# Kernel tuning notes

Hardware: AMD Instinct MI355X
Metric: run time of the kernel (lower is better)

The kernel has to match this reference:

```python
import jax, jax.numpy as jnp
import numpy as np

MARGIN = 2.0


def setup_inputs() -> dict:
    key = jax.random.key(0)
    k1, k2 = jax.random.split(key)
    predict = jax.random.normal(k1, (8192, 2048, 1, 1), dtype=jnp.float32)
    gt = jax.random.randint(k2, (8192, 1), 0, 751, dtype=jnp.int64)
    return {"predict": predict, "gt": gt}


def reference(predict, gt):
    # predict: [B, 2048, 1, 1] -> [B, D]
    p = predict.reshape(predict.shape[0], -1)
    b, d = p.shape
    # pairwise squared L2 distance / dim, via GEMM (||a||^2 + ||b||^2 - 2 a.b)
    sq = jnp.sum(p * p, axis=1)  # [B]
    d2 = (sq[:, None] + sq[None, :] - 2.0 * (p @ p.T))
    d2 = jnp.maximum(d2, 0.0) / d  # clamp tiny negatives from GEMM roundoff
    g = gt.reshape(-1)
    label = (g[:, None] == g[None, :]).astype(p.dtype)  # [B, B]
    term = label * d2 + (1.0 - label) * jax.nn.relu(MARGIN - d2)
    # original loop sums over j >= i (diagonal contributes 0: same label, dist 0)
    mask = jnp.triu(jnp.ones((b, b), dtype=bool))
    loss = jnp.sum(jnp.where(mask, term, 0.0))
    return 2.0 * loss / (b * (b - 1))
```

## Files before the change

### kernel.cpp

```cpp
#include <hip/hip_runtime.h>
#include <stdint.h>

#define NROWS 8192
#define DIM   2048
#define MARGIN 2.0f
#define SCALEQ (127.0f / 6.0f)
#define S2     ((6.0f / 127.0f) * (6.0f / 127.0f))

#define BT2     256
#define BKB     128
#define NKT     (DIM / BKB)
#define NT2     (NROWS / BT2)
#define NTILES2 (NT2 * (NT2 + 1) / 2)
#define NSPL    16
#define ABUF_B  32768
#define BUF_B   65536
#define HALF_B  16384

typedef __attribute__((ext_vector_type(4)))  int  int4v;
typedef __attribute__((ext_vector_type(16))) int  int16v;
typedef unsigned char uchar;

__device__ __forceinline__ void decode_tile(int bid, int* ti, int* tj) {
    float fn = (float)NT2 + 0.5f;
    int r = (int)(fn - sqrtf(fn * fn - 2.0f * (float)bid));
    if (r < 0) r = 0;
    if (r >= NT2) r = NT2 - 1;
    while ((r + 1) * NT2 - ((r + 1) * r) / 2 <= bid) ++r;
    while (r * NT2 - (r * (r - 1)) / 2 > bid) --r;
    *ti = r;
    *tj = r + (bid - (r * NT2 - (r * (r - 1)) / 2));
}

__device__ __forceinline__ uint pack4(float4 v) {
    int q0 = (int)__builtin_rintf(v.x * SCALEQ);
    int q1 = (int)__builtin_rintf(v.y * SCALEQ);
    int q2 = (int)__builtin_rintf(v.z * SCALEQ);
    int q3 = (int)__builtin_rintf(v.w * SCALEQ);
    q0 = min(max(q0, -127), 127); q1 = min(max(q1, -127), 127);
    q2 = min(max(q2, -127), 127); q3 = min(max(q3, -127), 127);
    return (uint)(q0 & 0xFF) | ((uint)(q1 & 0xFF) << 8) |
           ((uint)(q2 & 0xFF) << 16) | ((uint)(q3 & 0xFF) << 24);
}

__global__ __launch_bounds__(256) void prep_kernel(const float* __restrict__ p,
                                                   uchar* __restrict__ pb,
                                                   float* __restrict__ sq) {
    int row = blockIdx.x;
    int t = threadIdx.x;
    const float4* prow = (const float4*)(p + (size_t)row * DIM);
    uint* qrow = (uint*)(pb + (size_t)row * DIM);
    float4 a = prow[t];
    float4 b = prow[t + 256];
    float s = a.x * a.x + a.y * a.y + a.z * a.z + a.w * a.w
            + b.x * b.x + b.y * b.y + b.z * b.z + b.w * b.w;
    qrow[t] = pack4(a);
    qrow[t + 256] = pack4(b);
#pragma unroll
    for (int o = 32; o > 0; o >>= 1) s += __shfl_down(s, o, 64);
    __shared__ float wsums[4];
    int lane = t & 63, wvv = t >> 6;
    if (lane == 0) wsums[wvv] = s;
    __syncthreads();
    if (t == 0) sq[row] = wsums[0] + wsums[1] + wsums[2] + wsums[3];
}

__device__ __forceinline__ void stage_ht(const uchar* __restrict__ pb,
                                         uchar* lds, int t, int which,
                                         int ibase, int jbase, int tid) {
    if (t >= NKT) t -= 2;
    const int h = which & 1;
    const int row0 = ((which >= 2) ? jbase : ibase) + h * 128;
    const uchar* g0 = pb + (size_t)row0 * DIM + t * BKB;
    uchar* l0 = lds + (t & 1) * BUF_B + ((which >= 2) ? ABUF_B : 0) + h * HALF_B;
#pragma unroll
    for (int r = 0; r < 2; ++r) {
        int row = r * 64 + (tid >> 3);
        int c8 = (tid & 7) ^ ((tid >> 3) & 7);
        const uchar* g = g0 + (size_t)row * DIM + c8 * 16;
        uchar* l = l0 + r * 8192 + (tid >> 6) * 1024;
        __builtin_amdgcn_global_load_lds(
            (const __attribute__((address_space(1))) uint32_t*)g,
            (__attribute__((address_space(3))) uint32_t*)l, 16, 0, 0);
    }
}

#define BARF()   do { __builtin_amdgcn_s_barrier(); \
                      asm volatile("" ::: "memory"); } while (0)
#define WAITL()  asm volatile("s_waitcnt lgkmcnt(0)" ::: "memory")
#define WAITV8() asm volatile("s_waitcnt vmcnt(8)" ::: "memory")
#define WAITV6() asm volatile("s_waitcnt vmcnt(6)" ::: "memory")
#define WAITV0() asm volatile("s_waitcnt vmcnt(0)" ::: "memory")
#define PRIO1()  __builtin_amdgcn_s_setprio(1)
#define PRIO0()  __builtin_amdgcn_s_setprio(0)

#define READ_A(AB, MH)                                                         \
    _Pragma("unroll") for (int mt = 0; mt < 2; ++mt)                           \
    _Pragma("unroll") for (int s = 0; s < 4; ++s) {                            \
        int rl = wr * 128 + ((MH) * 2 + mt) * 32 + (lane & 31);                \
        af[mt][s] = *(const int4v*)&(AB)[rl * 128 +                            \
                     (((2 * s + kh) ^ (lane & 7)) * 16)];                      \
    }

#define READ_B(BB, NH)                                                         \
    _Pragma("unroll") for (int s = 0; s < 4; ++s) {                            \
        int rl = wc * 64 + (NH) * 32 + (lane & 31);                            \
        bf[NH][s] = *(const int4v*)&(BB)[rl * 128 +                            \
                     (((2 * s + kh) ^ (lane & 7)) * 16)];                      \
    }

#define MFMA_Q(MH, NH)                                                         \
    _Pragma("unroll") for (int mt = 0; mt < 2; ++mt)                           \
    _Pragma("unroll") for (int s = 0; s < 4; ++s)                              \
        acc[(MH) * 2 + mt][NH] = __builtin_amdgcn_mfma_i32_32x32x32_i8(        \
            af[mt][s], bf[NH][s], acc[(MH) * 2 + mt][NH], 0, 0, 0);

#define STEP_FULL(T, BUF)                                                      \
    {                                                                          \
        const uchar* Ab = &lds[(BUF) * BUF_B];                                 \
        const uchar* Bb = &lds[(BUF) * BUF_B + ABUF_B];                        \
        READ_A(Ab, 0);                                                         \
        READ_B(Bb, 0);                                                         \
        READ_B(Bb, 1);                                                         \
        PRIO1(); MFMA_Q(0, 0); MFMA_Q(0, 1); PRIO0();                          \
        READ_A(Ab, 1);                                                         \
        WAITL(); BARF();                                                       \
        stage_ht(pb, lds, (T) + 2, 2, ibase, jbase, tid);                      \
        stage_ht(pb, lds, (T) + 2, 3, ibase, jbase, tid);                      \
        stage_ht(pb, lds, (T) + 2, 0, ibase, jbase, tid);                      \
        stage_ht(pb, lds, (T) + 2, 1, ibase, jbase, tid);                      \
        PRIO1(); MFMA_Q(1, 0); MFMA_Q(1, 1); PRIO0();                          \
        WAITV8(); BARF();                                                      \
    }

#define STEP_HALF(T, BUF)                                                      \
    {                                                                          \
        const uchar* Ab = &lds[(BUF) * BUF_B];                                 \
        const uchar* Bb = &lds[(BUF) * BUF_B + ABUF_B];                        \
        _Pragma("unroll") for (int mt = 0; mt < 2; ++mt)                       \
        _Pragma("unroll") for (int s = 0; s < 4; ++s) {                        \
            int rl = wrh * 64 + mt * 32 + (lane & 31);                         \
            af[mt][s] = *(const int4v*)&Ab[rl * 128 +                          \
                         (((2 * s + kh) ^ (lane & 7)) * 16)];                  \
        }                                                                      \
        READ_B(Bb, 0);                                                         \
        READ_B(Bb, 1);                                                         \
        PRIO1();                                                               \
        _Pragma("unroll") for (int mt = 0; mt < 2; ++mt)                       \
        _Pragma("unroll") for (int s = 0; s < 4; ++s)                          \
            acc[mt][0] = __builtin_amdgcn_mfma_i32_32x32x32_i8(                \
                af[mt][s], bf[0][s], acc[mt][0], 0, 0, 0);                     \
        _Pragma("unroll") for (int mt = 0; mt < 2; ++mt)                       \
        _Pragma("unroll") for (int s = 0; s < 4; ++s)                          \
            acc[mt][1] = __builtin_amdgcn_mfma_i32_32x32x32_i8(                \
                af[mt][s], bf[1][s], acc[mt][1], 0, 0, 0);                     \
        PRIO0();                                                               \
        WAITL(); BARF();                                                       \
        stage_ht(pb, lds, (T) + 2, 0, ibase, jbase, tid);                      \
        stage_ht(pb, lds, (T) + 2, 2, ibase, jbase, tid);                      \
        stage_ht(pb, lds, (T) + 2, 3, ibase, jbase, tid);                      \
        WAITV6(); BARF();                                                      \
    }

__global__ __launch_bounds__(512) void tile2_kernel(
    const uchar* __restrict__ pb, const float* __restrict__ sq,
    const int* __restrict__ gt, double* __restrict__ accum) {

    __shared__ uchar lds[2 * BUF_B];
    __shared__ float wsum[8];

    const int bx = (int)blockIdx.x;
    const bool is_half = (bx < 2 * NSPL);
    int bid, hh = 0;
    if (is_half) { bid = bx >> 1; hh = bx & 1; }
    else { int f = bx - 2 * NSPL; bid = NSPL + ((f & 7) << 6) + (f >> 3); }

    int ti, tj;
    decode_tile(bid, &ti, &tj);

    const int tid = threadIdx.x;
    const int lane = tid & 63;
    const int kh = lane >> 5;
    const int wv = tid >> 6;
    const int wc = wv & 3;
    const int jbase = tj * BT2;
    const int ibase = ti * BT2 + (is_half ? hh * 128 : 0);

    const float invd = 1.0f / (float)DIM;
    float lsum = 0.f;

    if (!is_half) {
        const int wr = wv >> 2;
        int16v acc[4][2] = {};
        int4v af[2][4];
        int4v bf[2][4];

        stage_ht(pb, lds, 0, 2, ibase, jbase, tid);
        stage_ht(pb, lds, 0, 3, ibase, jbase, tid);
        stage_ht(pb, lds, 0, 0, ibase, jbase, tid);
        stage_ht(pb, lds, 0, 1, ibase, jbase, tid);
        stage_ht(pb, lds, 1, 2, ibase, jbase, tid);
        stage_ht(pb, lds, 1, 3, ibase, jbase, tid);
        stage_ht(pb, lds, 1, 0, ibase, jbase, tid);
        stage_ht(pb, lds, 1, 1, ibase, jbase, tid);
        WAITV8();
        BARF();

#pragma unroll 1
        for (int s0 = 0; s0 < NKT; s0 += 2) {
            STEP_FULL(s0, 0);
            STEP_FULL(s0 + 1, 1);
        }
        WAITV0();
        BARF();

        int j0 = jbase + wc * 64 + (lane & 31);
        float sqj[2]; int gj[2];
#pragma unroll
        for (int n = 0; n < 2; ++n) { int j = j0 + n * 32; sqj[n] = sq[j]; gj[n] = gt[j]; }
        const float wb = (ti != tj) ? 2.0f : 1.0f;
#pragma unroll
        for (int mi = 0; mi < 4; ++mi) {
#pragma unroll
            for (int q = 0; q < 4; ++q) {
#pragma unroll
                for (int rr = 0; rr < 4; ++rr) {
                    int i = ibase + wr * 128 + mi * 32 + rr + 8 * q + 4 * kh;
                    float sqi = sq[i];
                    int gi = gt[i];
#pragma unroll
                    for (int n = 0; n < 2; ++n) {
                        int j = j0 + n * 32;
                        float dot = S2 * (float)acc[mi][n][q * 4 + rr];
                        float d2 = fmaxf(sqi + sqj[n] - 2.0f * dot, 0.0f) * invd;
                        float term = (gi == gj[n]) ? d2 : fmaxf(MARGIN - d2, 0.0f);
                        float w = wb;
                        if (ti == tj && i == j) w = 2.0f;
                        lsum += w * term;
                    }
                }
            }
        }
    } else {
        const int wrh = wv >> 2;
        int16v acc[2][2] = {};
        int4v af[2][4];
        int4v bf[2][4];

        stage_ht(pb, lds, 0, 0, ibase, jbase, tid);
        stage_ht(pb, lds, 0, 2, ibase, jbase, tid);
        stage_ht(pb, lds, 0, 3, ibase, jbase, tid);
        stage_ht(pb, lds, 1, 0, ibase, jbase, tid);
        stage_ht(pb, lds, 1, 2, ibase, jbase, tid);
        stage_ht(pb, lds, 1, 3, ibase, jbase, tid);
        WAITV6();
        BARF();

#pragma unroll 1
        for (int s0 = 0; s0 < NKT; s0 += 2) {
            STEP_HALF(s0, 0);
            STEP_HALF(s0 + 1, 1);
        }
        WAITV0();
        BARF();

        int j0 = jbase + wc * 64 + (lane & 31);
        float sqj[2]; int gj[2];
#pragma unroll
        for (int n = 0; n < 2; ++n) { int j = j0 + n * 32; sqj[n] = sq[j]; gj[n] = gt[j]; }
        const float wb = (ti != tj) ? 2.0f : 1.0f;
#pragma unroll
        for (int mt = 0; mt < 2; ++mt) {
#pragma unroll
            for (int q = 0; q < 4; ++q) {
#pragma unroll
                for (int rr = 0; rr < 4; ++rr) {
                    int i = ibase + wrh * 64 + mt * 32 + rr + 8 * q + 4 * kh;
                    float sqi = sq[i];
                    int gi = gt[i];
#pragma unroll
                    for (int n = 0; n < 2; ++n) {
                        int j = j0 + n * 32;
                        float dot = S2 * (float)acc[mt][n][q * 4 + rr];
                        float d2 = fmaxf(sqi + sqj[n] - 2.0f * dot, 0.0f) * invd;
                        float term = (gi == gj[n]) ? d2 : fmaxf(MARGIN - d2, 0.0f);
                        float w = wb;
                        if (ti == tj && i == j) w = 2.0f;
                        lsum += w * term;
                    }
                }
            }
        }
    }

#pragma unroll
    for (int o = 32; o > 0; o >>= 1) lsum += __shfl_down(lsum, o, 64);
    if (lane == 0) wsum[wv] = lsum;
    __syncthreads();
    if (tid == 0) {
        float s = 0.f;
#pragma unroll
        for (int w = 0; w < 8; ++w) s += wsum[w];
        atomicAdd(accum, (double)s);
    }
}

__global__ void finalize_kernel(const double* __restrict__ accum,
                                float* __restrict__ out) {
    if (threadIdx.x == 0)
        out[0] = (float)(accum[0] * (1.0 / ((double)NROWS * (double)(NROWS - 1))));
}

extern "C" void kernel_launch(void* const* d_in, const int* in_sizes, int n_in,
                              void* d_out, int out_size, void* d_ws, size_t ws_size,
                              hipStream_t stream) {
    (void)in_sizes; (void)n_in; (void)out_size; (void)ws_size;
    const float* p = (const float*)d_in[0];
    const int* gt = (const int*)d_in[1];
    float* out = (float*)d_out;

    uchar* pb = (uchar*)d_ws;
    size_t off = (size_t)NROWS * DIM;
    float* sq = (float*)((char*)d_ws + off);
    off += (size_t)NROWS * sizeof(float);
    double* accum = (double*)((char*)d_ws + off);

    (void)hipMemsetAsync(accum, 0, sizeof(double), stream);
    prep_kernel<<<NROWS, 256, 0, stream>>>(p, pb, sq);
    tile2_kernel<<<2 * NSPL + 512, 512, 0, stream>>>(pb, sq, gt, accum);
    finalize_kernel<<<1, 64, 0, stream>>>(accum, out);
}
```

Baseline: 118.3 us.

## Use 4-wave blocks with 128x128 per-wave tiles and quarter-split diagonal tiles

The tile kernel moves from 8 waves per block (each computing 128x64 of the 256x256 tile) to 4 waves per block, each computing a 128x128 sub-tile with 16 accumulators. Register fragments are reused across a 2x2 MFMA sub-block order. The first 16 tiles are now split four ways into 64-row strips instead of two ways, and staging issues more loads per thread to match. This raises MFMA work per LDS read and cuts wave count, at the cost of heavy register pressure (launch_bounds 256,1), lower occupancy, and the removal of the setprio hints.

```diff
diff --git a/kernel.cpp b/kernel.cpp
--- a/kernel.cpp
+++ b/kernel.cpp
@@ -12,7 +12,7 @@
 #define NKT     (DIM / BKB)
 #define NT2     (NROWS / BT2)
 #define NTILES2 (NT2 * (NT2 + 1) / 2)
-#define NSPL    16
+#define NQ      16
 #define ABUF_B  32768
 #define BUF_B   65536
 #define HALF_B  16384
@@ -74,106 +74,126 @@
     const uchar* g0 = pb + (size_t)row0 * DIM + t * BKB;
     uchar* l0 = lds + (t & 1) * BUF_B + ((which >= 2) ? ABUF_B : 0) + h * HALF_B;
 #pragma unroll
-    for (int r = 0; r < 2; ++r) {
-        int row = r * 64 + (tid >> 3);
+    for (int r = 0; r < 4; ++r) {
+        int row = r * 32 + (tid >> 3);
         int c8 = (tid & 7) ^ ((tid >> 3) & 7);
         const uchar* g = g0 + (size_t)row * DIM + c8 * 16;
-        uchar* l = l0 + r * 8192 + (tid >> 6) * 1024;
+        uchar* l = l0 + r * 4096 + (tid >> 6) * 1024;
         __builtin_amdgcn_global_load_lds(
             (const __attribute__((address_space(1))) uint32_t*)g,
             (__attribute__((address_space(3))) uint32_t*)l, 16, 0, 0);
     }
 }
 
-#define BARF()   do { __builtin_amdgcn_s_barrier(); \
-                      asm volatile("" ::: "memory"); } while (0)
-#define WAITL()  asm volatile("s_waitcnt lgkmcnt(0)" ::: "memory")
-#define WAITV8() asm volatile("s_waitcnt vmcnt(8)" ::: "memory")
-#define WAITV6() asm volatile("s_waitcnt vmcnt(6)" ::: "memory")
-#define WAITV0() asm volatile("s_waitcnt vmcnt(0)" ::: "memory")
-#define PRIO1()  __builtin_amdgcn_s_setprio(1)
-#define PRIO0()  __builtin_amdgcn_s_setprio(0)
-
-#define READ_A(AB, MH)                                                         \
+__device__ __forceinline__ void stage_qA(const uchar* __restrict__ pb,
+                                         uchar* lds, int t, int ibase, int tid) {
+    if (t >= NKT) t -= 2;
+    const uchar* g0 = pb + (size_t)ibase * DIM + t * BKB;
+    uchar* l0 = lds + (t & 1) * BUF_B;
+#pragma unroll
+    for (int r = 0; r < 2; ++r) {
+        int row = r * 32 + (tid >> 3);
+        int c8 = (tid & 7) ^ ((tid >> 3) & 7);
+        const uchar* g = g0 + (size_t)row * DIM + c8 * 16;
+        uchar* l = l0 + r * 4096 + (tid >> 6) * 1024;
+        __builtin_amdgcn_global_load_lds(
+            (const __attribute__((address_space(1))) uint32_t*)g,
+            (__attribute__((address_space(3))) uint32_t*)l, 16, 0, 0);
+    }
+}
+
+#define BARF()    do { __builtin_amdgcn_s_barrier(); \
+                       asm volatile("" ::: "memory"); } while (0)
+#define WAITL()   asm volatile("s_waitcnt lgkmcnt(0)" ::: "memory")
+#define WAITV16() asm volatile("s_waitcnt vmcnt(16)" ::: "memory")
+#define WAITV10() asm volatile("s_waitcnt vmcnt(10)" ::: "memory")
+#define WAITV0()  asm volatile("s_waitcnt vmcnt(0)" ::: "memory")
+
+#define RD_A(DST, MH)                                                          \
     _Pragma("unroll") for (int mt = 0; mt < 2; ++mt)                           \
     _Pragma("unroll") for (int s = 0; s < 4; ++s) {                            \
-        int rl = wr * 128 + ((MH) * 2 + mt) * 32 + (lane & 31);                \
-        af[mt][s] = *(const int4v*)&(AB)[rl * 128 +                            \
-                     (((2 * s + kh) ^ (lane & 7)) * 16)];                      \
-    }
-
-#define READ_B(BB, NH)                                                         \
+        int rl = wr2 * 128 + ((MH) * 2 + mt) * 32 + (lane & 31);               \
+        DST[mt][s] = *(const int4v*)&Ab[rl * 128 +                             \
+                      (((2 * s + kh) ^ (lane & 7)) * 16)];                     \
+    }
+
+#define RD_B(DST, NH)                                                          \
+    _Pragma("unroll") for (int nt = 0; nt < 2; ++nt)                           \
     _Pragma("unroll") for (int s = 0; s < 4; ++s) {                            \
-        int rl = wc * 64 + (NH) * 32 + (lane & 31);                            \
-        bf[NH][s] = *(const int4v*)&(BB)[rl * 128 +                            \
-                     (((2 * s + kh) ^ (lane & 7)) * 16)];                      \
-    }
-
-#define MFMA_Q(MH, NH)                                                         \
+        int rl = wc2 * 128 + ((NH) * 2 + nt) * 32 + (lane & 31);               \
+        DST[nt][s] = *(const int4v*)&Bb[rl * 128 +                             \
+                      (((2 * s + kh) ^ (lane & 7)) * 16)];                     \
+    }
+
+#define MM(AF, BF, MH, NH)                                                     \
     _Pragma("unroll") for (int mt = 0; mt < 2; ++mt)                           \
+    _Pragma("unroll") for (int nt = 0; nt < 2; ++nt)                           \
     _Pragma("unroll") for (int s = 0; s < 4; ++s)                              \
-        acc[(MH) * 2 + mt][NH] = __builtin_amdgcn_mfma_i32_32x32x32_i8(        \
-            af[mt][s], bf[NH][s], acc[(MH) * 2 + mt][NH], 0, 0, 0);
+        acc[(MH) * 2 + mt][(NH) * 2 + nt] =                                    \
+            __builtin_amdgcn_mfma_i32_32x32x32_i8(                             \
+                AF[mt][s], BF[nt][s], acc[(MH) * 2 + mt][(NH) * 2 + nt],       \
+                0, 0, 0);
 
 #define STEP_FULL(T, BUF)                                                      \
     {                                                                          \
         const uchar* Ab = &lds[(BUF) * BUF_B];                                 \
         const uchar* Bb = &lds[(BUF) * BUF_B + ABUF_B];                        \
-        READ_A(Ab, 0);                                                         \
-        READ_B(Bb, 0);                                                         \
-        READ_B(Bb, 1);                                                         \
-        PRIO1(); MFMA_Q(0, 0); MFMA_Q(0, 1); PRIO0();                          \
-        READ_A(Ab, 1);                                                         \
+        RD_A(af0, 0); RD_B(bf0, 0);                                            \
+        RD_A(af1, 1);                                                          \
+        MM(af0, bf0, 0, 0);                                                    \
+        RD_B(bf1, 1);                                                          \
+        MM(af1, bf0, 1, 0);                                                    \
+        RD_A(af0, 0);              \
+        MM(af1, bf1, 1, 1);                                                    \
+        MM(af0, bf1, 0, 1);                                                    \
         WAITL(); BARF();                                                       \
         stage_ht(pb, lds, (T) + 2, 2, ibase, jbase, tid);                      \
         stage_ht(pb, lds, (T) + 2, 3, ibase, jbase, tid);                      \
         stage_ht(pb, lds, (T) + 2, 0, ibase, jbase, tid);                      \
         stage_ht(pb, lds, (T) + 2, 1, ibase, jbase, tid);                      \
-        PRIO1(); MFMA_Q(1, 0); MFMA_Q(1, 1); PRIO0();                          \
-        WAITV8(); BARF();                                                      \
-    }
-
-#define STEP_HALF(T, BUF)                                                      \
+        WAITV16(); BARF();                                                     \
+    }
+
+#define STEP_Q(T, BUF)                                                         \
     {                                                                          \
         const uchar* Ab = &lds[(BUF) * BUF_B];                                 \
         const uchar* Bb = &lds[(BUF) * BUF_B + ABUF_B];                        \
         _Pragma("unroll") for (int mt = 0; mt < 2; ++mt)                       \
         _Pragma("unroll") for (int s = 0; s < 4; ++s) {                        \
-            int rl = wrh * 64 + mt * 32 + (lane & 31);                         \
-            af[mt][s] = *(const int4v*)&Ab[rl * 128 +                          \
+            int rl = mt * 32 + (lane & 31);                                    \
+            aq[mt][s] = *(const int4v*)&Ab[rl * 128 +                          \
                          (((2 * s + kh) ^ (lane & 7)) * 16)];                  \
         }                                                                      \
-        READ_B(Bb, 0);                                                         \
-        READ_B(Bb, 1);                                                         \
-        PRIO1();                                                               \
+        _Pragma("unroll") for (int nt = 0; nt < 2; ++nt)                       \
+        _Pragma("unroll") for (int s = 0; s < 4; ++s) {                        \
+            int rl = wv * 64 + nt * 32 + (lane & 31);                          \
+            bq[nt][s] = *(const int4v*)&Bb[rl * 128 +                          \
+                         (((2 * s + kh) ^ (lane & 7)) * 16)];                  \
+        }                                                                      \
         _Pragma("unroll") for (int mt = 0; mt < 2; ++mt)                       \
+        _Pragma("unroll") for (int nt = 0; nt < 2; ++nt)                       \
         _Pragma("unroll") for (int s = 0; s < 4; ++s)                          \
-            acc[mt][0] = __builtin_amdgcn_mfma_i32_32x32x32_i8(                \
-                af[mt][s], bf[0][s], acc[mt][0], 0, 0, 0);                     \
-        _Pragma("unroll") for (int mt = 0; mt < 2; ++mt)                       \
-        _Pragma("unroll") for (int s = 0; s < 4; ++s)                          \
-            acc[mt][1] = __builtin_amdgcn_mfma_i32_32x32x32_i8(                \
-                af[mt][s], bf[1][s], acc[mt][1], 0, 0, 0);                     \
-        PRIO0();                                                               \
+            accq[mt][nt] = __builtin_amdgcn_mfma_i32_32x32x32_i8(              \
+                aq[mt][s], bq[nt][s], accq[mt][nt], 0, 0, 0);                  \
         WAITL(); BARF();                                                       \
-        stage_ht(pb, lds, (T) + 2, 0, ibase, jbase, tid);                      \
+        stage_qA(pb, lds, (T) + 2, ibase, tid);                                \
         stage_ht(pb, lds, (T) + 2, 2, ibase, jbase, tid);                      \
         stage_ht(pb, lds, (T) + 2, 3, ibase, jbase, tid);                      \
-        WAITV6(); BARF();                                                      \
-    }
-
-__global__ __launch_bounds__(512) void tile2_kernel(
+        WAITV10(); BARF();                                                     \
+    }
+
+__global__ __launch_bounds__(256, 1) void tile2_kernel(
     const uchar* __restrict__ pb, const float* __restrict__ sq,
     const int* __restrict__ gt, double* __restrict__ accum) {
 
     __shared__ uchar lds[2 * BUF_B];
-    __shared__ float wsum[8];
+    __shared__ float wsum[4];
 
     const int bx = (int)blockIdx.x;
-    const bool is_half = (bx < 2 * NSPL);
-    int bid, hh = 0;
-    if (is_half) { bid = bx >> 1; hh = bx & 1; }
-    else { int f = bx - 2 * NSPL; bid = NSPL + ((f & 7) << 6) + (f >> 3); }
+    const bool is_q = (bx < 4 * NQ);
+    int bid, qq = 0;
+    if (is_q) { bid = bx >> 2; qq = bx & 3; }
+    else { int f = bx - 4 * NQ; bid = NQ + ((f & 7) << 6) + (f >> 3); }
 
     int ti, tj;
     decode_tile(bid, &ti, &tj);
@@ -182,18 +202,17 @@
     const int lane = tid & 63;
     const int kh = lane >> 5;
     const int wv = tid >> 6;
-    const int wc = wv & 3;
+    const int wr2 = wv >> 1;
+    const int wc2 = wv & 1;
     const int jbase = tj * BT2;
-    const int ibase = ti * BT2 + (is_half ? hh * 128 : 0);
+    const int ibase = ti * BT2 + (is_q ? qq * 64 : 0);
 
     const float invd = 1.0f / (float)DIM;
     float lsum = 0.f;
 
-    if (!is_half) {
-        const int wr = wv >> 2;
-        int16v acc[4][2] = {};
-        int4v af[2][4];
-        int4v bf[2][4];
+    if (!is_q) {
+        int16v acc[4][4] = {};
+        int4v af0[2][4], af1[2][4], bf0[2][4], bf1[2][4];
 
         stage_ht(pb, lds, 0, 2, ibase, jbase, tid);
         stage_ht(pb, lds, 0, 3, ibase, jbase, tid);
@@ -203,7 +222,7 @@
         stage_ht(pb, lds, 1, 3, ibase, jbase, tid);
         stage_ht(pb, lds, 1, 0, ibase, jbase, tid);
         stage_ht(pb, lds, 1, 1, ibase, jbase, tid);
-        WAITV8();
+        WAITV16();
         BARF();
 
 #pragma unroll 1
@@ -214,10 +233,10 @@
         WAITV0();
         BARF();
 
-        int j0 = jbase + wc * 64 + (lane & 31);
-        float sqj[2]; int gj[2];
-#pragma unroll
-        for (int n = 0; n < 2; ++n) { int j = j0 + n * 32; sqj[n] = sq[j]; gj[n] = gt[j]; }
+        int j0 = jbase + wc2 * 128 + (lane & 31);
+        float sqj[4]; int gj[4];
+#pragma unroll
+        for (int nh = 0; nh < 4; ++nh) { int j = j0 + nh * 32; sqj[nh] = sq[j]; gj[nh] = gt[j]; }
         const float wb = (ti != tj) ? 2.0f : 1.0f;
 #pragma unroll
         for (int mi = 0; mi < 4; ++mi) {
@@ -225,15 +244,15 @@
             for (int q = 0; q < 4; ++q) {
 #pragma unroll
                 for (int rr = 0; rr < 4; ++rr) {
-                    int i = ibase + wr * 128 + mi * 32 + rr + 8 * q + 4 * kh;
+                    int i = ibase + wr2 * 128 + mi * 32 + rr + 8 * q + 4 * kh;
                     float sqi = sq[i];
                     int gi = gt[i];
 #pragma unroll
-                    for (int n = 0; n < 2; ++n) {
-                        int j = j0 + n * 32;
-                        float dot = S2 * (float)acc[mi][n][q * 4 + rr];
-                        float d2 = fmaxf(sqi + sqj[n] - 2.0f * dot, 0.0f) * invd;
-                        float term = (gi == gj[n]) ? d2 : fmaxf(MARGIN - d2, 0.0f);
+                    for (int nh = 0; nh < 4; ++nh) {
+                        int j = j0 + nh * 32;
+                        float dot = S2 * (float)acc[mi][nh][q * 4 + rr];
+                        float d2 = fmaxf(sqi + sqj[nh] - 2.0f * dot, 0.0f) * invd;
+                        float term = (gi == gj[nh]) ? d2 : fmaxf(MARGIN - d2, 0.0f);
                         float w = wb;
                         if (ti == tj && i == j) w = 2.0f;
                         lsum += w * term;
@@ -242,32 +261,30 @@
             }
         }
     } else {
-        const int wrh = wv >> 2;
-        int16v acc[2][2] = {};
-        int4v af[2][4];
-        int4v bf[2][4];
-
-        stage_ht(pb, lds, 0, 0, ibase, jbase, tid);
+        int16v accq[2][2] = {};
+        int4v aq[2][4], bq[2][4];
+
+        stage_qA(pb, lds, 0, ibase, tid);
         stage_ht(pb, lds, 0, 2, ibase, jbase, tid);
         stage_ht(pb, lds, 0, 3, ibase, jbase, tid);
-        stage_ht(pb, lds, 1, 0, ibase, jbase, tid);
+        stage_qA(pb, lds, 1, ibase, tid);
         stage_ht(pb, lds, 1, 2, ibase, jbase, tid);
         stage_ht(pb, lds, 1, 3, ibase, jbase, tid);
-        WAITV6();
+        WAITV10();
         BARF();
 
 #pragma unroll 1
         for (int s0 = 0; s0 < NKT; s0 += 2) {
-            STEP_HALF(s0, 0);
-            STEP_HALF(s0 + 1, 1);
+            STEP_Q(s0, 0);
+            STEP_Q(s0 + 1, 1);
         }
         WAITV0();
         BARF();
 
-        int j0 = jbase + wc * 64 + (lane & 31);
+        int j0 = jbase + wv * 64 + (lane & 31);
         float sqj[2]; int gj[2];
 #pragma unroll
-        for (int n = 0; n < 2; ++n) { int j = j0 + n * 32; sqj[n] = sq[j]; gj[n] = gt[j]; }
+        for (int nt = 0; nt < 2; ++nt) { int j = j0 + nt * 32; sqj[nt] = sq[j]; gj[nt] = gt[j]; }
         const float wb = (ti != tj) ? 2.0f : 1.0f;
 #pragma unroll
         for (int mt = 0; mt < 2; ++mt) {
@@ -275,15 +292,15 @@
             for (int q = 0; q < 4; ++q) {
 #pragma unroll
                 for (int rr = 0; rr < 4; ++rr) {
-                    int i = ibase + wrh * 64 + mt * 32 + rr + 8 * q + 4 * kh;
+                    int i = ibase + mt * 32 + rr + 8 * q + 4 * kh;
                     float sqi = sq[i];
                     int gi = gt[i];
 #pragma unroll
-                    for (int n = 0; n < 2; ++n) {
-                        int j = j0 + n * 32;
-                        float dot = S2 * (float)acc[mt][n][q * 4 + rr];
-                        float d2 = fmaxf(sqi + sqj[n] - 2.0f * dot, 0.0f) * invd;
-                        float term = (gi == gj[n]) ? d2 : fmaxf(MARGIN - d2, 0.0f);
+                    for (int nt = 0; nt < 2; ++nt) {
+                        int j = j0 + nt * 32;
+                        float dot = S2 * (float)accq[mt][nt][q * 4 + rr];
+                        float d2 = fmaxf(sqi + sqj[nt] - 2.0f * dot, 0.0f) * invd;
+                        float term = (gi == gj[nt]) ? d2 : fmaxf(MARGIN - d2, 0.0f);
                         float w = wb;
                         if (ti == tj && i == j) w = 2.0f;
                         lsum += w * term;
@@ -297,12 +314,8 @@
     for (int o = 32; o > 0; o >>= 1) lsum += __shfl_down(lsum, o, 64);
     if (lane == 0) wsum[wv] = lsum;
     __syncthreads();
-    if (tid == 0) {
-        float s = 0.f;
-#pragma unroll
-        for (int w = 0; w < 8; ++w) s += wsum[w];
-        atomicAdd(accum, (double)s);
-    }
+    if (tid == 0)
+        atomicAdd(accum, (double)(wsum[0] + wsum[1] + wsum[2] + wsum[3]));
 }
 
 __global__ void finalize_kernel(const double* __restrict__ accum,
@@ -327,6 +340,6 @@
 
     (void)hipMemsetAsync(accum, 0, sizeof(double), stream);
     prep_kernel<<<NROWS, 256, 0, stream>>>(p, pb, sq);
-    tile2_kernel<<<2 * NSPL + 512, 512, 0, stream>>>(pb, sq, gt, accum);
+    tile2_kernel<<<4 * NQ + 512, 256, 0, stream>>>(pb, sq, gt, accum);
     finalize_kernel<<<1, 64, 0, stream>>>(accum, out);
 }
```

Result: slower. 171.7 us (+45.1%).

## Split tail tiles into quarter blocks and interleave LDS reads with MFMAs

Applied to the files above, without the earlier changes.

The 16 tail tiles are now split into four 64-row quarter blocks instead of two halves. Each wave computes a 64x32 sub-tile, which spreads the tail work across more CUs to cut load imbalance. The main full-tile step is rescheduled with separate A/B fragment registers, partial lgkmcnt waits and sched_barriers, so LDS reads and global staging overlap with MFMA groups. The costs are more registers, more barriers per step, and more redundant B-tile staging for the quarter blocks.

```diff
diff --git a/kernel.cpp b/kernel.cpp
--- a/kernel.cpp
+++ b/kernel.cpp
@@ -12,7 +12,7 @@
 #define NKT     (DIM / BKB)
 #define NT2     (NROWS / BT2)
 #define NTILES2 (NT2 * (NT2 + 1) / 2)
-#define NSPL    16
+#define NQ      16
 #define ABUF_B  32768
 #define BUF_B   65536
 #define HALF_B  16384
@@ -85,81 +85,105 @@
     }
 }
 
+__device__ __forceinline__ void stage_qA(const uchar* __restrict__ pb,
+                                         uchar* lds, int t, int ibase, int tid) {
+    if (t >= NKT) t -= 2;
+    const uchar* g0 = pb + (size_t)ibase * DIM + t * BKB;
+    uchar* l0 = lds + (t & 1) * BUF_B;
+    int row = tid >> 3;
+    int c8 = (tid & 7) ^ ((tid >> 3) & 7);
+    const uchar* g = g0 + (size_t)row * DIM + c8 * 16;
+    uchar* l = l0 + (tid >> 6) * 1024;
+    __builtin_amdgcn_global_load_lds(
+        (const __attribute__((address_space(1))) uint32_t*)g,
+        (__attribute__((address_space(3))) uint32_t*)l, 16, 0, 0);
+}
+
 #define BARF()   do { __builtin_amdgcn_s_barrier(); \
                       asm volatile("" ::: "memory"); } while (0)
-#define WAITL()  asm volatile("s_waitcnt lgkmcnt(0)" ::: "memory")
+#define WLG4()   asm volatile("s_waitcnt lgkmcnt(4)" ::: "memory")
+#define WLG0()   asm volatile("s_waitcnt lgkmcnt(0)" ::: "memory")
 #define WAITV8() asm volatile("s_waitcnt vmcnt(8)" ::: "memory")
-#define WAITV6() asm volatile("s_waitcnt vmcnt(6)" ::: "memory")
+#define WAITV5() asm volatile("s_waitcnt vmcnt(5)" ::: "memory")
 #define WAITV0() asm volatile("s_waitcnt vmcnt(0)" ::: "memory")
 #define PRIO1()  __builtin_amdgcn_s_setprio(1)
 #define PRIO0()  __builtin_amdgcn_s_setprio(0)
-
-#define READ_A(AB, MH)                                                         \
+#define SB0()    __builtin_amdgcn_sched_barrier(0)
+
+#define RD_A(DST, MH)                                                          \
     _Pragma("unroll") for (int mt = 0; mt < 2; ++mt)                           \
     _Pragma("unroll") for (int s = 0; s < 4; ++s) {                            \
         int rl = wr * 128 + ((MH) * 2 + mt) * 32 + (lane & 31);                \
-        af[mt][s] = *(const int4v*)&(AB)[rl * 128 +                            \
-                     (((2 * s + kh) ^ (lane & 7)) * 16)];                      \
-    }
-
-#define READ_B(BB, NH)                                                         \
+        DST[mt][s] = *(const int4v*)&Ab[rl * 128 +                             \
+                      (((2 * s + kh) ^ (lane & 7)) * 16)];                     \
+    }
+
+#define RD_B(DST, NH)                                                          \
     _Pragma("unroll") for (int s = 0; s < 4; ++s) {                            \
         int rl = wc * 64 + (NH) * 32 + (lane & 31);                            \
-        bf[NH][s] = *(const int4v*)&(BB)[rl * 128 +                            \
-                     (((2 * s + kh) ^ (lane & 7)) * 16)];                      \
-    }
-
-#define MFMA_Q(MH, NH)                                                         \
+        DST[s] = *(const int4v*)&Bb[rl * 128 +                                 \
+                  (((2 * s + kh) ^ (lane & 7)) * 16)];                         \
+    }
+
+#define MFMA_QR(AF, BF, MH, NH, S0, S1)                                        \
+    _Pragma("unroll") for (int s = (S0); s < (S1); ++s)                        \
     _Pragma("unroll") for (int mt = 0; mt < 2; ++mt)                           \
-    _Pragma("unroll") for (int s = 0; s < 4; ++s)                              \
         acc[(MH) * 2 + mt][NH] = __builtin_amdgcn_mfma_i32_32x32x32_i8(        \
-            af[mt][s], bf[NH][s], acc[(MH) * 2 + mt][NH], 0, 0, 0);
+            AF[mt][s], BF[s], acc[(MH) * 2 + mt][NH], 0, 0, 0);
 
 #define STEP_FULL(T, BUF)                                                      \
     {                                                                          \
         const uchar* Ab = &lds[(BUF) * BUF_B];                                 \
         const uchar* Bb = &lds[(BUF) * BUF_B + ABUF_B];                        \
-        READ_A(Ab, 0);                                                         \
-        READ_B(Bb, 0);                                                         \
-        READ_B(Bb, 1);                                                         \
-        PRIO1(); MFMA_Q(0, 0); MFMA_Q(0, 1); PRIO0();                          \
-        READ_A(Ab, 1);                                                         \
-        WAITL(); BARF();                                                       \
+        RD_A(af0, 0); RD_B(bf0, 0);                                            \
+        SB0();                                                                 \
+        RD_B(bf1, 1);                                                          \
+        WLG4(); SB0();                                                         \
+        PRIO1(); MFMA_QR(af0, bf0, 0, 0, 0, 4); PRIO0();                       \
+        WLG0(); SB0();                                                         \
+        PRIO1(); MFMA_QR(af0, bf1, 0, 1, 0, 2); PRIO0();                       \
+        SB0();                                                                 \
+        RD_A(af1, 1);                                                          \
+        PRIO1(); MFMA_QR(af0, bf1, 0, 1, 2, 4); PRIO0();                       \
+        BARF();                                                                \
         stage_ht(pb, lds, (T) + 2, 2, ibase, jbase, tid);                      \
         stage_ht(pb, lds, (T) + 2, 3, ibase, jbase, tid);                      \
+        WLG0(); SB0();                                                         \
+        PRIO1(); MFMA_QR(af1, bf0, 1, 0, 0, 4); PRIO0();                       \
+        BARF();                                                                \
         stage_ht(pb, lds, (T) + 2, 0, ibase, jbase, tid);                      \
         stage_ht(pb, lds, (T) + 2, 1, ibase, jbase, tid);                      \
-        PRIO1(); MFMA_Q(1, 0); MFMA_Q(1, 1); PRIO0();                          \
+        PRIO1(); MFMA_QR(af1, bf1, 1, 1, 0, 4); PRIO0();                       \
         WAITV8(); BARF();                                                      \
     }
 
-#define STEP_HALF(T, BUF)                                                      \
+#define STEP_Q(T, BUF)                                                         \
     {                                                                          \
         const uchar* Ab = &lds[(BUF) * BUF_B];                                 \
         const uchar* Bb = &lds[(BUF) * BUF_B + ABUF_B];                        \
         _Pragma("unroll") for (int mt = 0; mt < 2; ++mt)                       \
         _Pragma("unroll") for (int s = 0; s < 4; ++s) {                        \
-            int rl = wrh * 64 + mt * 32 + (lane & 31);                         \
-            af[mt][s] = *(const int4v*)&Ab[rl * 128 +                          \
+            int rl = mt * 32 + (lane & 31);                                    \
+            aq[mt][s] = *(const int4v*)&Ab[rl * 128 +                          \
                          (((2 * s + kh) ^ (lane & 7)) * 16)];                  \
         }                                                                      \
-        READ_B(Bb, 0);                                                         \
-        READ_B(Bb, 1);                                                         \
+        _Pragma("unroll") for (int s = 0; s < 4; ++s) {                        \
+            int rl = wv * 32 + (lane & 31);                                    \
+            bq[s] = *(const int4v*)&Bb[rl * 128 +                              \
+                     (((2 * s + kh) ^ (lane & 7)) * 16)];                      \
+        }                                                                      \
+        WLG0(); SB0();                                                         \
         PRIO1();                                                               \
+        _Pragma("unroll") for (int s = 0; s < 4; ++s)                          \
         _Pragma("unroll") for (int mt = 0; mt < 2; ++mt)                       \
-        _Pragma("unroll") for (int s = 0; s < 4; ++s)                          \
-            acc[mt][0] = __builtin_amdgcn_mfma_i32_32x32x32_i8(                \
-                af[mt][s], bf[0][s], acc[mt][0], 0, 0, 0);                     \
-        _Pragma("unroll") for (int mt = 0; mt < 2; ++mt)                       \
-        _Pragma("unroll") for (int s = 0; s < 4; ++s)                          \
-            acc[mt][1] = __builtin_amdgcn_mfma_i32_32x32x32_i8(                \
-                af[mt][s], bf[1][s], acc[mt][1], 0, 0, 0);                     \
+            accq[mt] = __builtin_amdgcn_mfma_i32_32x32x32_i8(                  \
+                aq[mt][s], bq[s], accq[mt], 0, 0, 0);                          \
         PRIO0();                                                               \
-        WAITL(); BARF();                                                       \
-        stage_ht(pb, lds, (T) + 2, 0, ibase, jbase, tid);                      \
+        BARF();                                                                \
+        stage_qA(pb, lds, (T) + 2, ibase, tid);                                \
         stage_ht(pb, lds, (T) + 2, 2, ibase, jbase, tid);                      \
         stage_ht(pb, lds, (T) + 2, 3, ibase, jbase, tid);                      \
-        WAITV6(); BARF();                                                      \
+        WAITV5(); BARF();                                                      \
     }
 
 __global__ __launch_bounds__(512) void tile2_kernel(
@@ -170,10 +194,10 @@
     __shared__ float wsum[8];
 
     const int bx = (int)blockIdx.x;
-    const bool is_half = (bx < 2 * NSPL);
-    int bid, hh = 0;
-    if (is_half) { bid = bx >> 1; hh = bx & 1; }
-    else { int f = bx - 2 * NSPL; bid = NSPL + ((f & 7) << 6) + (f >> 3); }
+    const bool is_q = (bx < 4 * NQ);
+    int bid, qq = 0;
+    if (is_q) { bid = bx >> 2; qq = bx & 3; }
+    else { int f = bx - 4 * NQ; bid = NQ + ((f & 7) << 6) + (f >> 3); }
 
     int ti, tj;
     decode_tile(bid, &ti, &tj);
@@ -182,18 +206,18 @@
     const int lane = tid & 63;
     const int kh = lane >> 5;
     const int wv = tid >> 6;
+    const int wr = wv >> 2;
     const int wc = wv & 3;
     const int jbase = tj * BT2;
-    const int ibase = ti * BT2 + (is_half ? hh * 128 : 0);
+    const int ibase = ti * BT2 + (is_q ? qq * 64 : 0);
 
     const float invd = 1.0f / (float)DIM;
     float lsum = 0.f;
 
-    if (!is_half) {
-        const int wr = wv >> 2;
+    if (!is_q) {
         int16v acc[4][2] = {};
-        int4v af[2][4];
-        int4v bf[2][4];
+        int4v af0[2][4], af1[2][4];
+        int4v bf0[4], bf1[4];
 
         stage_ht(pb, lds, 0, 2, ibase, jbase, tid);
         stage_ht(pb, lds, 0, 3, ibase, jbase, tid);
@@ -242,32 +266,29 @@
             }
         }
     } else {
-        const int wrh = wv >> 2;
-        int16v acc[2][2] = {};
-        int4v af[2][4];
-        int4v bf[2][4];
-
-        stage_ht(pb, lds, 0, 0, ibase, jbase, tid);
+        int16v accq[2] = {};
+        int4v aq[2][4], bq[4];
+
+        stage_qA(pb, lds, 0, ibase, tid);
         stage_ht(pb, lds, 0, 2, ibase, jbase, tid);
         stage_ht(pb, lds, 0, 3, ibase, jbase, tid);
-        stage_ht(pb, lds, 1, 0, ibase, jbase, tid);
+        stage_qA(pb, lds, 1, ibase, tid);
         stage_ht(pb, lds, 1, 2, ibase, jbase, tid);
         stage_ht(pb, lds, 1, 3, ibase, jbase, tid);
-        WAITV6();
+        WAITV5();
         BARF();
 
 #pragma unroll 1
         for (int s0 = 0; s0 < NKT; s0 += 2) {
-            STEP_HALF(s0, 0);
-            STEP_HALF(s0 + 1, 1);
+            STEP_Q(s0, 0);
+            STEP_Q(s0 + 1, 1);
         }
         WAITV0();
         BARF();
 
-        int j0 = jbase + wc * 64 + (lane & 31);
-        float sqj[2]; int gj[2];
-#pragma unroll
-        for (int n = 0; n < 2; ++n) { int j = j0 + n * 32; sqj[n] = sq[j]; gj[n] = gt[j]; }
+        int j = jbase + wv * 32 + (lane & 31);
+        float sqj = sq[j];
+        int gj = gt[j];
         const float wb = (ti != tj) ? 2.0f : 1.0f;
 #pragma unroll
         for (int mt = 0; mt < 2; ++mt) {
@@ -275,19 +296,13 @@
             for (int q = 0; q < 4; ++q) {
 #pragma unroll
                 for (int rr = 0; rr < 4; ++rr) {
-                    int i = ibase + wrh * 64 + mt * 32 + rr + 8 * q + 4 * kh;
-                    float sqi = sq[i];
-                    int gi = gt[i];
-#pragma unroll
-                    for (int n = 0; n < 2; ++n) {
-                        int j = j0 + n * 32;
-                        float dot = S2 * (float)acc[mt][n][q * 4 + rr];
-                        float d2 = fmaxf(sqi + sqj[n] - 2.0f * dot, 0.0f) * invd;
-                        float term = (gi == gj[n]) ? d2 : fmaxf(MARGIN - d2, 0.0f);
-                        float w = wb;
-                        if (ti == tj && i == j) w = 2.0f;
-                        lsum += w * term;
-                    }
+                    int i = ibase + mt * 32 + rr + 8 * q + 4 * kh;
+                    float dot = S2 * (float)accq[mt][q * 4 + rr];
+                    float d2 = fmaxf(sq[i] + sqj - 2.0f * dot, 0.0f) * invd;
+                    float term = (gt[i] == gj) ? d2 : fmaxf(MARGIN - d2, 0.0f);
+                    float w = wb;
+                    if (ti == tj && i == j) w = 2.0f;
+                    lsum += w * term;
                 }
             }
         }
@@ -327,6 +342,6 @@
 
     (void)hipMemsetAsync(accum, 0, sizeof(double), stream);
     prep_kernel<<<NROWS, 256, 0, stream>>>(p, pb, sq);
-    tile2_kernel<<<2 * NSPL + 512, 512, 0, stream>>>(pb, sq, gt, accum);
+    tile2_kernel<<<4 * NQ + 512, 512, 0, stream>>>(pb, sq, gt, accum);
     finalize_kernel<<<1, 64, 0, stream>>>(accum, out);
 }
```

Result: faster. 112.7 us (-4.7%).
